# Kernel optimization log

Hardware: AMD Instinct MI355X
Metric: run time of the kernel (lower is better)

The kernel has to match this reference:

```python
import jax, jax.numpy as jnp
import numpy as np

D_MODEL = 1024
NUM_HEADS = 16
D_K = D_MODEL // NUM_HEADS
BATCH = 2
SEQ = 2048


def setup_inputs() -> dict:
    key = jax.random.key(0)
    ks = jax.random.split(key, 9)
    s = 1.0 / np.sqrt(D_MODEL)
    X = jax.random.normal(ks[0], (BATCH, SEQ, D_MODEL), dtype=jnp.float32)
    # causal mask, broadcastable over batch and heads; 0 means masked
    mask = jnp.tril(jnp.ones((SEQ, SEQ), dtype=jnp.int32))[None, None]
    W_Q = jax.random.uniform(ks[1], (D_MODEL, D_MODEL), jnp.float32, -s, s)
    b_Q = jax.random.uniform(ks[2], (D_MODEL,), jnp.float32, -s, s)
    W_K = jax.random.uniform(ks[3], (D_MODEL, D_MODEL), jnp.float32, -s, s)
    b_K = jax.random.uniform(ks[4], (D_MODEL,), jnp.float32, -s, s)
    W_V = jax.random.uniform(ks[5], (D_MODEL, D_MODEL), jnp.float32, -s, s)
    b_V = jax.random.uniform(ks[6], (D_MODEL,), jnp.float32, -s, s)
    W_O = jax.random.uniform(ks[7], (D_MODEL, D_MODEL), jnp.float32, -s, s)
    b_O = jax.random.uniform(ks[8], (D_MODEL,), jnp.float32, -s, s)
    return {"X": X, "mask": mask, "W_Q": W_Q, "b_Q": b_Q, "W_K": W_K,
            "b_K": b_K, "W_V": W_V, "b_V": b_V, "W_O": W_O, "b_O": b_O}


def reference(X, mask, W_Q, b_Q, W_K, b_K, W_V, b_V, W_O, b_O):
    B, S, _ = X.shape
    H, Dk = NUM_HEADS, D_K
    # projections; torch Linear uses y = x @ W.T + b; here W_* is stored as [in, out]
    Q = (X @ W_Q + b_Q).reshape(B, S, H, Dk).transpose(0, 2, 1, 3)  # [B,H,S,Dk]
    K = (X @ W_K + b_K).reshape(B, S, H, Dk).transpose(0, 2, 1, 3)
    V = (X @ W_V + b_V).reshape(B, S, H, Dk).transpose(0, 2, 1, 3)
    scores = jnp.einsum("bhqd,bhkd->bhqk", Q, K) / jnp.sqrt(jnp.asarray(Dk, X.dtype))
    scores = jnp.where(mask == 0, -jnp.inf, scores)
    attn = jax.nn.softmax(scores, axis=-1)  # [B,H,S,S]
    out = jnp.einsum("bhqk,bhkd->bhqd", attn, V)
    out = out.transpose(0, 2, 1, 3).reshape(B, S, H * Dk)
    return out @ W_O + b_O
```

## Files before the change

kernel.cpp:

```cpp
#include <hip/hip_runtime.h>
#include <math.h>

#define S_LEN 2048
#define DM 1024
#define NH 16
#define DK 64
#define BB 2
#define MROWS (BB * S_LEN)
#define QTILES (S_LEN / 64)
#define LOG2E 1.44269504088896340736f

typedef __attribute__((ext_vector_type(8))) short bf16x8;
typedef __attribute__((ext_vector_type(4))) float f32x4;

__device__ __forceinline__ unsigned short f2bf(float f) {
    unsigned int u = __builtin_bit_cast(unsigned int, f);
    u += 0x7fff + ((u >> 16) & 1);
    return (unsigned short)(u >> 16);
}

__device__ __forceinline__ float hw_exp2(float x) {
    return __builtin_amdgcn_exp2f(x);
}

__device__ __forceinline__ void gload_lds16(const unsigned short* g, unsigned short* l) {
    __builtin_amdgcn_global_load_lds(
        (const __attribute__((address_space(1))) unsigned int*)(const void*)g,
        (__attribute__((address_space(3))) unsigned int*)(void*)l, 16, 0, 0);
}

__global__ __launch_bounds__(256) void prep_kernel(
    const float* __restrict__ X, unsigned short* __restrict__ Xb,
    const float* __restrict__ W_Q, const float* __restrict__ W_K,
    const float* __restrict__ W_V, const float* __restrict__ W_O,
    unsigned short* __restrict__ WqkvT, unsigned short* __restrict__ WoT) {
    const int z = blockIdx.z;
    if (z == 0) {
        int i = (blockIdx.x * 256 + threadIdx.x) * 4;
        float4 v = *(const float4*)(X + i);
        ushort4 o;
        o.x = f2bf(v.x); o.y = f2bf(v.y); o.z = f2bf(v.z); o.w = f2bf(v.w);
        *(ushort4*)(Xb + i) = o;
        return;
    }
    if (blockIdx.x >= (DM / 64) * (DM / 64)) return;
    const float* in = z == 1 ? W_Q : (z == 2 ? W_K : (z == 3 ? W_V : W_O));
    unsigned short* out = z == 4 ? WoT : (WqkvT + (size_t)(z - 1) * DM * DM);
    __shared__ float tile[64][65];
    const int bx = blockIdx.x & 15, by = blockIdx.x >> 4;
    const int tx = threadIdx.x & 63, ty = threadIdx.x >> 6;
#pragma unroll
    for (int i = 0; i < 64; i += 4)
        tile[ty + i][tx] = in[(size_t)(by * 64 + ty + i) * DM + bx * 64 + tx];
    __syncthreads();
#pragma unroll
    for (int i = 0; i < 64; i += 4)
        out[(size_t)(bx * 64 + ty + i) * DM + by * 64 + tx] = f2bf(tile[tx][ty + i]);
}

#define VMCNT(N) asm volatile("s_waitcnt vmcnt(" #N ")" ::: "memory")

#define QPHASE(MH_, NH_, PRESTAGE, PREWAIT) do {                               \
    bf16x8 af_[4][2], bf_[2][2];                                               \
    _Pragma("unroll") for (int ii = 0; ii < 4; ++ii)                           \
    _Pragma("unroll") for (int kk = 0; kk < 2; ++kk)                           \
        af_[ii][kk] = *(const bf16x8*)&As[(MH_) * 8192 +                       \
            (ii * 16 + ln + wm * 64) * 64 + (((kk * 4 + lq) ^ (ln & 7)) * 8)]; \
    _Pragma("unroll") for (int jj = 0; jj < 2; ++jj)                           \
    _Pragma("unroll") for (int kk = 0; kk < 2; ++kk)                           \
        bf_[jj][kk] = *(const bf16x8*)&Bs[(NH_) * 8192 +                       \
            (jj * 16 + ln + wn * 32) * 64 + (((kk * 4 + lq) ^ (ln & 7)) * 8)]; \
    PRESTAGE;                                                                  \
    __builtin_amdgcn_s_barrier();                                              \
    asm volatile("s_waitcnt lgkmcnt(0)" ::: "memory");                         \
    __builtin_amdgcn_sched_barrier(0);                                         \
    __builtin_amdgcn_s_setprio(1);                                             \
    _Pragma("unroll") for (int kk = 0; kk < 2; ++kk)                           \
    _Pragma("unroll") for (int ii = 0; ii < 4; ++ii)                           \
    _Pragma("unroll") for (int jj = 0; jj < 2; ++jj)                           \
        acc[(MH_) * 4 + ii][(NH_) * 2 + jj] =                                  \
            __builtin_amdgcn_mfma_f32_16x16x32_bf16(                           \
                af_[ii][kk], bf_[jj][kk],                                      \
                acc[(MH_) * 4 + ii][(NH_) * 2 + jj], 0, 0, 0);                 \
    __builtin_amdgcn_s_setprio(0);                                             \
    PREWAIT;                                                                   \
    __builtin_amdgcn_s_barrier();                                              \
} while (0)

__global__ __launch_bounds__(512, 2) void gemm_qkv_kernel(
    const unsigned short* __restrict__ A,
    const unsigned short* __restrict__ Bt,
    const float* __restrict__ bQ, const float* __restrict__ bK,
    const float* __restrict__ bV,
    unsigned short* __restrict__ outQ, unsigned short* __restrict__ outK,
    unsigned short* __restrict__ outV) {
    __shared__ __align__(16) unsigned short smem[65536];
    const int tid = threadIdx.x;
    const int wave = tid >> 6, lane = tid & 63;
    const int lq = lane >> 4, ln = lane & 15;
    const int wm = wave >> 2, wn = wave & 3;
    const int m0 = blockIdx.y * 256, n0 = blockIdx.x * 256;

    f32x4 acc[8][4];
#pragma unroll
    for (int i = 0; i < 8; ++i)
#pragma unroll
        for (int j = 0; j < 4; ++j) acc[i][j] = (f32x4){0.f, 0.f, 0.f, 0.f};

    auto stageA = [&](int t, int h) {
#pragma unroll
        for (int s = 0; s < 2; ++s) {
            int p = (s << 9) + tid;
            int rp = p >> 3;
            int grow = (rp & 63) + ((rp >> 6) << 7) + (h << 6);
            gload_lds16(A + (size_t)(m0 + grow) * DM + (t << 6) +
                            (((tid & 7) ^ (rp & 7)) << 3),
                        smem + ((t & 1) << 14) + (h << 13) + (p << 3));
        }
    };
    auto stageB = [&](int t, int h) {
#pragma unroll
        for (int s = 0; s < 2; ++s) {
            int p = (s << 9) + tid;
            int rp = p >> 3;
            int grow = (rp & 31) + ((rp >> 5) << 6) + (h << 5);
            gload_lds16(Bt + (size_t)(n0 + grow) * DM + (t << 6) +
                            (((tid & 7) ^ (rp & 7)) << 3),
                        smem + 32768 + ((t & 1) << 14) + (h << 13) + (p << 3));
        }
    };

    stageB(0, 0); stageA(0, 0); stageA(0, 1); stageB(0, 1);
    stageB(1, 0); stageA(1, 0);
    VMCNT(4);
    __builtin_amdgcn_s_barrier();

    for (int t = 0; t < 14; ++t) {
        const unsigned short* As = smem + ((t & 1) << 14);
        const unsigned short* Bs = smem + 32768 + ((t & 1) << 14);
        QPHASE(0, 0, stageA(t + 1, 1), (void)0);
        QPHASE(1, 0, stageB(t + 1, 1), VMCNT(6));
        QPHASE(0, 1, stageB(t + 2, 0), (void)0);
        QPHASE(1, 1, stageA(t + 2, 0), VMCNT(6));
    }
    {
        const unsigned short* As = smem;
        const unsigned short* Bs = smem + 32768;
        QPHASE(0, 0, stageA(15, 1), (void)0);
        QPHASE(1, 0, stageB(15, 1), VMCNT(6));
        QPHASE(0, 1, (void)0, (void)0);
        QPHASE(1, 1, (void)0, VMCNT(2));
    }
    {
        const unsigned short* As = smem + 16384;
        const unsigned short* Bs = smem + 32768 + 16384;
        QPHASE(0, 0, (void)0, (void)0);
        QPHASE(1, 0, (void)0, VMCNT(0));
        QPHASE(0, 1, (void)0, (void)0);
        QPHASE(1, 1, (void)0, (void)0);
    }

    const int which = n0 >> 10;
    const float* bias = which == 0 ? bQ : (which == 1 ? bK : bV);
    const float scale = which == 0 ? 0.125f * LOG2E : 1.0f;
    unsigned short* ob = which == 0 ? outQ : (which == 1 ? outK : outV);
    unsigned short* Ts = smem + wave * 4608;
    const int nb = (n0 & 1023) + wn * 64;
    const int hh = nb >> 6;
    const int bI = (m0 + wm * 128) >> 11;
    const int sb = (m0 + wm * 128) & 2047;
#pragma unroll
    for (int ih = 0; ih < 2; ++ih) {
#pragma unroll
        for (int i2 = 0; i2 < 4; ++i2)
#pragma unroll
            for (int j = 0; j < 4; ++j)
#pragma unroll
                for (int r = 0; r < 4; ++r) {
                    int rl = i2 * 16 + lq * 4 + r;
                    int cl = j * 16 + ln;
                    float v = (acc[ih * 4 + i2][j][r] + bias[nb + cl]) * scale;
                    if (which == 2) Ts[cl * 72 + rl] = f2bf(v);
                    else            Ts[rl * 72 + cl] = f2bf(v);
                }
        const int sfull = sb + ih * 64;
        if (which <= 1) {
            unsigned short* dst = ob + ((size_t)(bI * NH + hh) * S_LEN + sfull) * DK;
#pragma unroll
            for (int t8 = 0; t8 < 8; ++t8) {
                int rl = t8 * 8 + (lane >> 3);
                *(uint4*)(dst + rl * DK + (lane & 7) * 8) =
                    *(const uint4*)&Ts[rl * 72 + (lane & 7) * 8];
            }
        } else {
            unsigned short* dst = ob + ((size_t)(bI * NH + hh) * DK) * S_LEN + sfull;
#pragma unroll
            for (int t8 = 0; t8 < 8; ++t8) {
                int dkl = t8 * 8 + (lane >> 3);
                *(uint4*)(dst + (size_t)dkl * S_LEN + (lane & 7) * 8) =
                    *(const uint4*)&Ts[dkl * 72 + (lane & 7) * 8];
            }
        }
    }
}

__global__ __launch_bounds__(256) void gemm_o_kernel(
    const unsigned short* __restrict__ A,
    const unsigned short* __restrict__ Bt,
    const float* __restrict__ bias,
    float* __restrict__ out_f) {
    const int K = DM;
    __shared__ __align__(16) unsigned short smem[2 * 6144];
    const int tid = threadIdx.x;
    const int wave = tid >> 6, lane = tid & 63;
    const int lq = lane >> 4, ln = lane & 15;
    const int m0 = blockIdx.y * 128, n0 = blockIdx.x * 64;
    const int wr = (wave >> 1) * 64, wc = (wave & 1) * 32;

    f32x4 acc[4][2];
#pragma unroll
    for (int i = 0; i < 4; ++i)
#pragma unroll
        for (int j = 0; j < 2; ++j)
            acc[i][j] = (f32x4){0.f, 0.f, 0.f, 0.f};

    const unsigned short* ga = A  + (size_t)(m0 + (tid >> 2)) * K + (tid & 3) * 8;
    const unsigned short* gb = Bt + (size_t)(n0 + (tid >> 2)) * K + (tid & 3) * 8;
    const size_t half = (size_t)64 * K;

    {
        unsigned short* An = smem;
        gload_lds16(ga, An + tid * 8);
        gload_lds16(ga + half, An + 2048 + tid * 8);
        gload_lds16(gb, An + 4096 + tid * 8);
    }

    for (int k0 = 0; k0 < K; k0 += 32) {
        const int cur = (k0 >> 5) & 1;
        unsigned short* As = smem + cur * 6144;
        unsigned short* Bs = As + 4096;
        __syncthreads();
        if (k0 + 32 < K) {
            unsigned short* An = smem + (cur ^ 1) * 6144;
            gload_lds16(ga + k0 + 32, An + tid * 8);
            gload_lds16(ga + half + k0 + 32, An + 2048 + tid * 8);
            gload_lds16(gb + k0 + 32, An + 4096 + tid * 8);
        }
        bf16x8 af[4], bfv[2];
#pragma unroll
        for (int i = 0; i < 4; ++i) af[i]  = *(const bf16x8*)&As[(wr + i * 16 + ln) * 32 + lq * 8];
#pragma unroll
        for (int j = 0; j < 2; ++j) bfv[j] = *(const bf16x8*)&Bs[(wc + j * 16 + ln) * 32 + lq * 8];
#pragma unroll
        for (int i = 0; i < 4; ++i)
#pragma unroll
            for (int j = 0; j < 2; ++j)
                acc[i][j] = __builtin_amdgcn_mfma_f32_16x16x32_bf16(af[i], bfv[j], acc[i][j], 0, 0, 0);
    }

#pragma unroll
    for (int i = 0; i < 4; ++i)
#pragma unroll
        for (int j = 0; j < 2; ++j)
#pragma unroll
            for (int r = 0; r < 4; ++r) {
                int m = m0 + wr + i * 16 + lq * 4 + r;
                int n = n0 + wc + j * 16 + ln;
                out_f[(size_t)m * DM + n] = acc[i][j][r] + bias[n];
            }
}

__global__ __launch_bounds__(512, 4) void attn_kernel(
    const unsigned short* __restrict__ Qg,
    const unsigned short* __restrict__ Kg,
    const unsigned short* __restrict__ Vg,
    unsigned short* __restrict__ Og) {
    __shared__ __align__(16) unsigned short KBUF[2 * 128 * 64];
    __shared__ __align__(16) unsigned short VBUF[2 * 64 * 128];
    __shared__ __align__(16) unsigned short Pw[8 * 640];

    const int tid = threadIdx.x;
    const int wave = tid >> 6, lane = tid & 63;
    const int lq = lane >> 4, ln = lane & 15;
    const int bh = blockIdx.x, b = bh >> 4, h = bh & 15;
    const int j = blockIdx.y;
    const int grp = wave >> 2, wv = wave & 3;
    const int qt = grp == 0 ? (QTILES - 1 - j) : j;
    const int nkv_me = grp == 0 ? ((33 - j) >> 1) : ((j + 2) >> 1);
    const int T = (33 - j) >> 1;

    const unsigned short* Qb = Qg + (size_t)bh * S_LEN * DK;
    const unsigned short* Kb = Kg + (size_t)bh * S_LEN * DK;
    const unsigned short* Vb = Vg + (size_t)bh * DK * S_LEN;

    const int krow_l = lane >> 3;
    const int kchunk = (lane & 7) ^ krow_l;
    const int vrow_l = lane >> 4;

    {
#pragma unroll
        for (int s = 0; s < 2; ++s)
            gload_lds16(Kb + (size_t)(wave * 16 + s * 8 + krow_l) * DK + kchunk * 8,
                        KBUF + (wave * 16 + s * 8) * 64 + lane * 8);
#pragma unroll
        for (int s = 0; s < 2; ++s) {
            int rv = wave * 8 + s * 4 + vrow_l;
            int c  = (lane & 15) ^ (rv & 15);
            gload_lds16(Vb + (size_t)rv * S_LEN + c * 8,
                        VBUF + (wave * 8 + s * 4) * 128 + lane * 8);
        }
    }

    const int q0 = qt * 64;
    bf16x8 qf0 = *(const bf16x8*)(Qb + (q0 + wv * 16 + ln) * DK + lq * 8);
    bf16x8 qf1 = *(const bf16x8*)(Qb + (q0 + wv * 16 + ln) * DK + 32 + lq * 8);

    const short one_bf = (short)0x3F80;
    const bf16x8 onesf = {one_bf, one_bf, one_bf, one_bf,
                          one_bf, one_bf, one_bf, one_bf};

    f32x4 oacc[4];
    f32x4 lacc = (f32x4){0.f, 0.f, 0.f, 0.f};
#pragma unroll
    for (int i = 0; i < 4; ++i) oacc[i] = (f32x4){0.f, 0.f, 0.f, 0.f};

    for (int g = 0; g < T; ++g) {
        const int cur = g & 1;
        unsigned short* Kl = KBUF + cur * 8192;
        unsigned short* Vl = VBUF + cur * 8192;
        __syncthreads();

        if (g + 1 < T) {
            const int kv0n = (g + 1) * 128;
            unsigned short* Kn = KBUF + (cur ^ 1) * 8192;
            unsigned short* Vn = VBUF + (cur ^ 1) * 8192;
#pragma unroll
            for (int s = 0; s < 2; ++s)
                gload_lds16(Kb + (size_t)(kv0n + wave * 16 + s * 8 + krow_l) * DK + kchunk * 8,
                            Kn + (wave * 16 + s * 8) * 64 + lane * 8);
#pragma unroll
            for (int s = 0; s < 2; ++s) {
                int rv = wave * 8 + s * 4 + vrow_l;
                int c  = (lane & 15) ^ (rv & 15);
                gload_lds16(Vb + (size_t)rv * S_LEN + kv0n + c * 8,
                            Vn + (wave * 8 + s * 4) * 128 + lane * 8);
            }
        }

        if (g < nkv_me) {
            const int kv0 = g * 128;

            f32x4 sc[8];
#pragma unroll
            for (int ct = 0; ct < 8; ++ct) {
                const int rbase = (ct * 16 + ln) * 64;
                bf16x8 k0 = *(const bf16x8*)&Kl[rbase + ((lq ^ (ln & 7)) * 8)];
                bf16x8 k1 = *(const bf16x8*)&Kl[rbase + (((lq + 4) ^ (ln & 7)) * 8)];
                f32x4 a = (f32x4){0.f, 0.f, 0.f, 0.f};
                a = __builtin_amdgcn_mfma_f32_16x16x32_bf16(qf0, k0, a, 0, 0, 0);
                a = __builtin_amdgcn_mfma_f32_16x16x32_bf16(qf1, k1, a, 0, 0, 0);
                sc[ct] = a;
            }

            if (g == nkv_me - 1) {
#pragma unroll
                for (int ct = 0; ct < 8; ++ct) {
                    int col = kv0 + ct * 16 + ln;
#pragma unroll
                    for (int r = 0; r < 4; ++r) {
                        int row = q0 + wv * 16 + lq * 4 + r;
                        if (col > row) sc[ct][r] = -INFINITY;
                    }
                }
            }

#pragma unroll
            for (int ct = 0; ct < 8; ++ct)
#pragma unroll
                for (int r = 0; r < 4; ++r)
                    sc[ct][r] = hw_exp2(sc[ct][r]);

            unsigned short* Pq = Pw + wave * 640;
#pragma unroll
            for (int qd = 0; qd < 4; ++qd) {
#pragma unroll
                for (int c2 = 0; c2 < 2; ++c2)
#pragma unroll
                    for (int r = 0; r < 4; ++r)
                        Pq[(lq * 4 + r) * 40 + c2 * 16 + ln] = f2bf(sc[qd * 2 + c2][r]);
                bf16x8 pf = *(const bf16x8*)&Pq[ln * 40 + lq * 8];
                lacc = __builtin_amdgcn_mfma_f32_16x16x32_bf16(pf, onesf, lacc, 0, 0, 0);
#pragma unroll
                for (int dkt = 0; dkt < 4; ++dkt) {
                    const unsigned short* vr =
                        &Vl[(dkt * 16 + ln) * 128 + (((qd * 4 + lq) ^ ln) * 8)];
                    oacc[dkt] = __builtin_amdgcn_mfma_f32_16x16x32_bf16(pf, *(const bf16x8*)vr, oacc[dkt], 0, 0, 0);
                }
            }
        }
    }

#pragma unroll
    for (int r = 0; r < 4; ++r) {
        float inv = 1.0f / lacc[r];
        int s = q0 + wv * 16 + lq * 4 + r;
#pragma unroll
        for (int dkt = 0; dkt < 4; ++dkt)
            Og[((size_t)(b * S_LEN + s)) * DM + h * 64 + dkt * 16 + ln] =
                f2bf(oacc[dkt][r] * inv);
    }
}

extern "C" void kernel_launch(void* const* d_in, const int* in_sizes, int n_in,
                              void* d_out, int out_size, void* d_ws, size_t ws_size,
                              hipStream_t stream) {
    const float* X   = (const float*)d_in[0];
    const float* W_Q = (const float*)d_in[2];
    const float* b_Q = (const float*)d_in[3];
    const float* W_K = (const float*)d_in[4];
    const float* b_K = (const float*)d_in[5];
    const float* W_V = (const float*)d_in[6];
    const float* b_V = (const float*)d_in[7];
    const float* W_O = (const float*)d_in[8];
    const float* b_O = (const float*)d_in[9];

    unsigned short* Xb    = (unsigned short*)d_ws;
    unsigned short* WqkvT = Xb    + (size_t)MROWS * DM;
    unsigned short* WoT   = WqkvT + (size_t)3 * DM * DM;
    unsigned short* Qb    = WoT   + (size_t)DM * DM;
    unsigned short* Kb    = Qb    + (size_t)MROWS * DM;
    unsigned short* Vtb   = Kb    + (size_t)MROWS * DM;
    unsigned short* Ob    = Vtb   + (size_t)MROWS * DM;

    prep_kernel<<<dim3((MROWS * DM) / 1024, 1, 5), 256, 0, stream>>>(
        X, Xb, W_Q, W_K, W_V, W_O, WqkvT, WoT);

    gemm_qkv_kernel<<<dim3(3 * DM / 256, MROWS / 256), 512, 0, stream>>>(
        Xb, WqkvT, b_Q, b_K, b_V, Qb, Kb, Vtb);

    attn_kernel<<<dim3(BB * NH, QTILES / 2), 512, 0, stream>>>(Qb, Kb, Vtb, Ob);

    gemm_o_kernel<<<dim3(DM / 64, MROWS / 128), 256, 0, stream>>>(
        Ob, WoT, b_O, (float*)d_out);
}
```

Baseline: 191.5 us.

## Software-pipeline LDS fragment reads across phases in QKV GEMM with register reuse

Restructures the QKV projection GEMM main loop so A/B fragments are read from LDS one phase ahead into persistent registers (aX/aY/b0/b1), reusing loaded fragments across two MFMA phases in a snake order. The lgkmcnt(0) wait before each MFMA block goes away, so LDS reads overlap with matrix ops and fewer fragment reloads are needed. In exchange it raises register pressure, which matters under launch_bounds(512,2), and it changes the vmcnt wait counts and the staging order, which the correctness of the smem hazards depends on.

```diff
diff --git a/kernel.cpp b/kernel.cpp
--- a/kernel.cpp
+++ b/kernel.cpp
@@ -60,30 +60,39 @@
 
 #define VMCNT(N) asm volatile("s_waitcnt vmcnt(" #N ")" ::: "memory")
 
-#define QPHASE(MH_, NH_, PRESTAGE, PREWAIT) do {                               \
-    bf16x8 af_[4][2], bf_[2][2];                                               \
+#define RD_A(DST_, BASE_, MH_) do {                                            \
     _Pragma("unroll") for (int ii = 0; ii < 4; ++ii)                           \
     _Pragma("unroll") for (int kk = 0; kk < 2; ++kk)                           \
-        af_[ii][kk] = *(const bf16x8*)&As[(MH_) * 8192 +                       \
+        DST_[ii][kk] = *(const bf16x8*)&(BASE_)[(MH_) * 8192 +                 \
             (ii * 16 + ln + wm * 64) * 64 + (((kk * 4 + lq) ^ (ln & 7)) * 8)]; \
+} while (0)
+
+#define RD_B(DST_, BASE_, NH_) do {                                            \
     _Pragma("unroll") for (int jj = 0; jj < 2; ++jj)                           \
     _Pragma("unroll") for (int kk = 0; kk < 2; ++kk)                           \
-        bf_[jj][kk] = *(const bf16x8*)&Bs[(NH_) * 8192 +                       \
+        DST_[jj][kk] = *(const bf16x8*)&(BASE_)[(NH_) * 8192 +                 \
             (jj * 16 + ln + wn * 32) * 64 + (((kk * 4 + lq) ^ (ln & 7)) * 8)]; \
-    PRESTAGE;                                                                  \
-    __builtin_amdgcn_s_barrier();                                              \
-    asm volatile("s_waitcnt lgkmcnt(0)" ::: "memory");                         \
-    __builtin_amdgcn_sched_barrier(0);                                         \
-    __builtin_amdgcn_s_setprio(1);                                             \
+} while (0)
+
+#define MMQ(MH_, NH_, AR_, BR_) do {                                           \
     _Pragma("unroll") for (int kk = 0; kk < 2; ++kk)                           \
     _Pragma("unroll") for (int ii = 0; ii < 4; ++ii)                           \
     _Pragma("unroll") for (int jj = 0; jj < 2; ++jj)                           \
         acc[(MH_) * 4 + ii][(NH_) * 2 + jj] =                                  \
             __builtin_amdgcn_mfma_f32_16x16x32_bf16(                           \
-                af_[ii][kk], bf_[jj][kk],                                      \
+                AR_[ii][kk], BR_[jj][kk],                                      \
                 acc[(MH_) * 4 + ii][(NH_) * 2 + jj], 0, 0, 0);                 \
+} while (0)
+
+#define PH(PRE_, MM_, POST_) do {                                              \
+    PRE_;                                                                      \
+    __builtin_amdgcn_sched_barrier(0);                                         \
+    __builtin_amdgcn_s_barrier();                                              \
+    __builtin_amdgcn_sched_barrier(0);                                         \
+    __builtin_amdgcn_s_setprio(1);                                             \
+    MM_;                                                                       \
     __builtin_amdgcn_s_setprio(0);                                             \
-    PREWAIT;                                                                   \
+    POST_;                                                                     \
     __builtin_amdgcn_s_barrier();                                              \
 } while (0)
 
@@ -130,34 +139,50 @@
         }
     };
 
-    stageB(0, 0); stageA(0, 0); stageA(0, 1); stageB(0, 1);
+    bf16x8 aX[4][2], aY[4][2], b0[2][2], b1[2][2];
+
+    stageB(0, 0); stageA(0, 0); stageB(0, 1); stageA(0, 1);
     stageB(1, 0); stageA(1, 0);
-    VMCNT(4);
+    VMCNT(8);
     __builtin_amdgcn_s_barrier();
-
-    for (int t = 0; t < 14; ++t) {
-        const unsigned short* As = smem + ((t & 1) << 14);
-        const unsigned short* Bs = smem + 32768 + ((t & 1) << 14);
-        QPHASE(0, 0, stageA(t + 1, 1), (void)0);
-        QPHASE(1, 0, stageB(t + 1, 1), VMCNT(6));
-        QPHASE(0, 1, stageB(t + 2, 0), (void)0);
-        QPHASE(1, 1, stageA(t + 2, 0), VMCNT(6));
-    }
     {
         const unsigned short* As = smem;
         const unsigned short* Bs = smem + 32768;
-        QPHASE(0, 0, stageA(15, 1), (void)0);
-        QPHASE(1, 0, stageB(15, 1), VMCNT(6));
-        QPHASE(0, 1, (void)0, (void)0);
-        QPHASE(1, 1, (void)0, VMCNT(2));
+        RD_A(aX, As, 0);
+        RD_B(b0, Bs, 0);
+    }
+    VMCNT(4);
+    __builtin_amdgcn_s_barrier();
+
+    for (int t = 0; t < 14; ++t) {
+        const unsigned short* Asc = smem + ((t & 1) << 14);
+        const unsigned short* Bsc = smem + 32768 + ((t & 1) << 14);
+        const unsigned short* Asn = smem + (((t + 1) & 1) << 14);
+        const unsigned short* Bsn = smem + 32768 + (((t + 1) & 1) << 14);
+        PH(RD_B(b1, Bsc, 1); stageA(t + 1, 1), MMQ(0, 0, aX, b0), (void)0);
+        PH(RD_A(aY, Asc, 1); stageB(t + 1, 1), MMQ(0, 1, aX, b1), VMCNT(4));
+        PH(RD_A(aX, Asn, 0); stageB(t + 2, 0), MMQ(1, 1, aY, b1), (void)0);
+        PH(stageA(t + 2, 0),                   MMQ(1, 0, aY, b0),
+           RD_B(b0, Bsn, 0); VMCNT(4));
     }
     {
-        const unsigned short* As = smem + 16384;
-        const unsigned short* Bs = smem + 32768 + 16384;
-        QPHASE(0, 0, (void)0, (void)0);
-        QPHASE(1, 0, (void)0, VMCNT(0));
-        QPHASE(0, 1, (void)0, (void)0);
-        QPHASE(1, 1, (void)0, (void)0);
+        const unsigned short* Asc = smem;
+        const unsigned short* Bsc = smem + 32768;
+        const unsigned short* Asn = smem + 16384;
+        const unsigned short* Bsn = smem + 32768 + 16384;
+        PH(RD_B(b1, Bsc, 1); stageA(15, 1), MMQ(0, 0, aX, b0), (void)0);
+        PH(RD_A(aY, Asc, 1); stageB(15, 1), MMQ(0, 1, aX, b1), VMCNT(4));
+        PH(RD_A(aX, Asn, 0),                MMQ(1, 1, aY, b1), (void)0);
+        PH((void)0,                         MMQ(1, 0, aY, b0),
+           RD_B(b0, Bsn, 0); VMCNT(0));
+    }
+    {
+        const unsigned short* Asc = smem + 16384;
+        const unsigned short* Bsc = smem + 32768 + 16384;
+        PH(RD_B(b1, Bsc, 1), MMQ(0, 0, aX, b0), (void)0);
+        PH(RD_A(aY, Asc, 1), MMQ(0, 1, aX, b1), (void)0);
+        PH((void)0,          MMQ(1, 1, aY, b1), (void)0);
+        PH((void)0,          MMQ(1, 0, aY, b0), (void)0);
     }
 
     const int which = n0 >> 10;
```

Result: no change. 188.9 us (-1.3%).
